# Optimization experiments

Measured on AMD Instinct MI355X. Metric: run time of the kernel, lower is better.

## Reference

```python
import jax, jax.numpy as jnp
import numpy as np

BN_EPS = 1e-3  # Keras BatchNormalization default epsilon
K = 7          # kernel_size


def setup_inputs() -> dict:
    key = jax.random.key(0)
    ks = jax.random.split(key, 5)
    B, L, C, F = 128, 512, 128, 128
    L_out = L - K + 1  # 506, valid padding, stride 1
    x = jax.random.normal(ks[0], (B, L, C), dtype=jnp.float32)
    # LocallyConnected1D unshared weights: (L_out, K*C, F), lecun_normal ~ N(0, 1/fan_in)
    kernel = jax.random.normal(ks[1], (L_out, K * C, F), dtype=jnp.float32) * (1.0 / np.sqrt(K * C))
    bias = jnp.zeros((L_out, F), dtype=jnp.float32)
    gamma = jnp.ones((F,), dtype=jnp.float32)
    beta = jnp.zeros((F,), dtype=jnp.float32)
    moving_mean = jax.random.normal(ks[2], (F,), dtype=jnp.float32) * 0.1
    moving_var = jax.random.uniform(ks[3], (F,), dtype=jnp.float32, minval=0.5, maxval=1.5)
    return {"x": x, "kernel": kernel, "bias": bias, "gamma": gamma,
            "beta": beta, "moving_mean": moving_mean, "moving_var": moving_var}


def _local_block(x, kernel, bias, gamma, beta, moving_mean, moving_var):
    B, L, C = x.shape
    L_out = L - K + 1
    F = kernel.shape[-1]
    # Patch extraction: idx[l, k] = l + k -> patches (B, L_out, K, C)
    idx = jnp.arange(L_out)[:, None] + jnp.arange(K)[None, :]
    patches = x[:, idx, :]                                  # (B, L_out, K, C)
    w = kernel.reshape(L_out, K, C, F)                      # unshared per-position weights
    y = jnp.einsum('blkc,lkcf->blf', patches, w) + bias     # (B, L_out, F)
    # BatchNorm (inference, axis=-1) fused with affine
    inv = gamma * jax.lax.rsqrt(moving_var + BN_EPS)
    y = y * inv + (beta - moving_mean * inv)
    return jax.nn.relu(y)


def reference(x, kernel, bias, gamma, beta, moving_mean, moving_var):
    return _local_block(x, kernel, bias, gamma, beta, moving_mean, moving_var)
```

## Files before the change

### kernel.cpp

```cpp
#include <hip/hip_runtime.h>

#define LO 506
#define LL 512
#define CC 128
#define FF 128
#define KC 896
#define BK 32
#define NK 28
#define XS 40
#define WS 40

typedef __attribute__((ext_vector_type(8))) short short8;
typedef __attribute__((ext_vector_type(4))) float floatx4;
typedef __attribute__((ext_vector_type(4))) unsigned int uintx4;
typedef unsigned short ushort_t;

static __device__ __forceinline__ ushort_t f2bf(float f) {
    union { float f; unsigned int u; } c; c.f = f;
    unsigned int u = c.u;
    return (ushort_t)((u + 0x7fffu + ((u >> 16) & 1u)) >> 16);
}
static __device__ __forceinline__ unsigned int pk2(float a, float b) {
    return (unsigned int)f2bf(a) | ((unsigned int)f2bf(b) << 16);
}

__global__ __launch_bounds__(512, 4)
void local_block_kernel(const float* __restrict__ x,
                        const float* __restrict__ wg,
                        const float* __restrict__ bias,
                        const float* __restrict__ gamma,
                        const float* __restrict__ beta,
                        const float* __restrict__ mmean,
                        const float* __restrict__ mvar,
                        float* __restrict__ out)
{
    const int l    = blockIdx.x;
    const int t    = threadIdx.x;
    const int lane = t & 63;
    const int wave = t >> 6;
    const int q    = lane >> 4;
    const int l16  = lane & 15;
    const int wr   = wave >> 1;
    const int wc   = wave & 1;

    __shared__ __align__(16) ushort_t Xs[128 * XS];
    __shared__ __align__(16) ushort_t Wt[128 * WS];

    const int am  = t >> 2;
    const int ak0 = (t & 3) * 8;
    const float* aptr = x + (size_t)am * (LL * CC) + l * CC + ak0;
    ushort_t* asd = &Xs[am * XS + ak0];

    const int wf  = t & 127;
    const int wk  = (t >> 7) * 8;
    const float* wptr = wg + (size_t)l * (KC * FF) + wf;
    ushort_t* wsd = &Wt[wf * WS + wk];

    floatx4 acc[2][4] = {};

    floatx4 areg[2];
    float   wreg[8];

#define LOAD_A(KT) { const float* p = aptr + (KT) * BK;                         \
        areg[0] = *(const floatx4*)(p);                                         \
        areg[1] = *(const floatx4*)(p + 4); }

#define LOAD_W(KT) { const float* p = wptr + (size_t)((KT) * BK + wk) * FF;     \
        _Pragma("unroll") for (int j = 0; j < 8; ++j)                           \
            wreg[j] = __builtin_nontemporal_load(p + j * FF); }

    LOAD_A(0); LOAD_W(0);

    for (int kt = 0; kt < NK; ++kt) {
        __syncthreads();
        {
            uintx4 av = { pk2(areg[0].x, areg[0].y),
                          pk2(areg[0].z, areg[0].w),
                          pk2(areg[1].x, areg[1].y),
                          pk2(areg[1].z, areg[1].w) };
            *(uintx4*)asd = av;
        }
        {
            uintx4 wv = { pk2(wreg[0], wreg[1]),
                          pk2(wreg[2], wreg[3]),
                          pk2(wreg[4], wreg[5]),
                          pk2(wreg[6], wreg[7]) };
            *(uintx4*)wsd = wv;
        }
        __syncthreads();
        if (kt + 1 < NK) { LOAD_A(kt + 1); LOAD_W(kt + 1); }
        short8 af[2], bfr[4];
#pragma unroll
        for (int mi = 0; mi < 2; ++mi)
            af[mi] = *(const short8*)&Xs[(wr*32 + mi*16 + l16) * XS + q*8];
#pragma unroll
        for (int ni = 0; ni < 4; ++ni)
            bfr[ni] = *(const short8*)&Wt[(wc*64 + ni*16 + l16) * WS + q*8];
#pragma unroll
        for (int mi = 0; mi < 2; ++mi)
#pragma unroll
            for (int ni = 0; ni < 4; ++ni)
                acc[mi][ni] = __builtin_amdgcn_mfma_f32_16x16x32_bf16(
                    af[mi], bfr[ni], acc[mi][ni], 0, 0, 0);
    }

#pragma unroll
    for (int ni = 0; ni < 4; ++ni) {
        int f = wc*64 + ni*16 + l16;
        float inv = gamma[f] * rsqrtf(mvar[f] + 1e-3f);
        float off = bias[l * FF + f] * inv + beta[f] - mmean[f] * inv;
#pragma unroll
        for (int mi = 0; mi < 2; ++mi) {
#pragma unroll
            for (int rg = 0; rg < 4; ++rg) {
                int b = wr*32 + mi*16 + q*4 + rg;
                float v = acc[mi][ni][rg] * inv + off;
                __builtin_nontemporal_store(fmaxf(v, 0.0f),
                    &out[((size_t)b * LO + l) * FF + f]);
            }
        }
    }
#undef LOAD_A
#undef LOAD_W
}

extern "C" void kernel_launch(void* const* d_in, const int* in_sizes, int n_in,
                              void* d_out, int out_size, void* d_ws, size_t ws_size,
                              hipStream_t stream) {
    const float* x     = (const float*)d_in[0];
    const float* w     = (const float*)d_in[1];
    const float* bias  = (const float*)d_in[2];
    const float* gamma = (const float*)d_in[3];
    const float* beta  = (const float*)d_in[4];
    const float* mmean = (const float*)d_in[5];
    const float* mvar  = (const float*)d_in[6];
    float* out = (float*)d_out;

    local_block_kernel<<<dim3(LO), dim3(512), 0, stream>>>(
        x, w, bias, gamma, beta, mmean, mvar, out);
}
```

Baseline: 361.1 us.

## Double-buffer LDS tiles with two-deep register prefetch and XCD-aware block remap

Switches to two LDS buffers and two register prefetch sets, so global loads for tile k+2 are in flight while tile k is computed. This leaves one barrier per k-step instead of two. It also remaps block IDs so that consecutive positions l land on the same XCD, which should improve L2 sharing of the overlapping x rows. The cost is more registers and twice the LDS, which may reduce occupancy. The barrier relies on the alternating buffers to avoid write-after-read hazards.

```diff
diff --git a/kernel.cpp b/kernel.cpp
--- a/kernel.cpp
+++ b/kernel.cpp
@@ -34,7 +34,14 @@
                         const float* __restrict__ mvar,
                         float* __restrict__ out)
 {
-    const int l    = blockIdx.x;
+    const int bid = blockIdx.x;
+    const int xcd = bid & 7;
+    const int idx = bid >> 3;
+    const int q8  = LO >> 3;
+    const int r8  = LO & 7;
+    const int l   = (xcd < r8) ? xcd * (q8 + 1) + idx
+                               : r8 * (q8 + 1) + (xcd - r8) * q8 + idx;
+
     const int t    = threadIdx.x;
     const int lane = t & 63;
     const int wave = t >> 6;
@@ -43,65 +50,66 @@
     const int wr   = wave >> 1;
     const int wc   = wave & 1;
 
-    __shared__ __align__(16) ushort_t Xs[128 * XS];
-    __shared__ __align__(16) ushort_t Wt[128 * WS];
+    __shared__ __align__(16) ushort_t Xs[2][128 * XS];
+    __shared__ __align__(16) ushort_t Wt[2][128 * WS];
 
     const int am  = t >> 2;
     const int ak0 = (t & 3) * 8;
     const float* aptr = x + (size_t)am * (LL * CC) + l * CC + ak0;
-    ushort_t* asd = &Xs[am * XS + ak0];
 
     const int wf  = t & 127;
     const int wk  = (t >> 7) * 8;
     const float* wptr = wg + (size_t)l * (KC * FF) + wf;
-    ushort_t* wsd = &Wt[wf * WS + wk];
 
     floatx4 acc[2][4] = {};
 
-    floatx4 areg[2];
-    float   wreg[8];
+    floatx4 areg0[2], areg1[2];
+    float   wreg0[8], wreg1[8];
 
-#define LOAD_A(KT) { const float* p = aptr + (KT) * BK;                         \
-        areg[0] = *(const floatx4*)(p);                                         \
-        areg[1] = *(const floatx4*)(p + 4); }
+#define LOAD_A(AR, KT) { const float* p = aptr + (KT) * BK;                     \
+        AR[0] = *(const floatx4*)(p);                                           \
+        AR[1] = *(const floatx4*)(p + 4); }
 
-#define LOAD_W(KT) { const float* p = wptr + (size_t)((KT) * BK + wk) * FF;     \
+#define LOAD_W(WR, KT) { const float* p = wptr + (size_t)((KT) * BK + wk) * FF; \
         _Pragma("unroll") for (int j = 0; j < 8; ++j)                           \
-            wreg[j] = __builtin_nontemporal_load(p + j * FF); }
+            WR[j] = __builtin_nontemporal_load(p + j * FF); }
 
-    LOAD_A(0); LOAD_W(0);
+#define STAGE(S, AR, WR) {                                                      \
+        uintx4 av = { pk2(AR[0].x, AR[0].y), pk2(AR[0].z, AR[0].w),             \
+                      pk2(AR[1].x, AR[1].y), pk2(AR[1].z, AR[1].w) };           \
+        *(uintx4*)&Xs[S][am * XS + ak0] = av;                                   \
+        uintx4 wv = { pk2(WR[0], WR[1]), pk2(WR[2], WR[3]),                     \
+                      pk2(WR[4], WR[5]), pk2(WR[6], WR[7]) };                   \
+        *(uintx4*)&Wt[S][wf * WS + wk] = wv; }
 
-    for (int kt = 0; kt < NK; ++kt) {
-        __syncthreads();
-        {
-            uintx4 av = { pk2(areg[0].x, areg[0].y),
-                          pk2(areg[0].z, areg[0].w),
-                          pk2(areg[1].x, areg[1].y),
-                          pk2(areg[1].z, areg[1].w) };
-            *(uintx4*)asd = av;
-        }
-        {
-            uintx4 wv = { pk2(wreg[0], wreg[1]),
-                          pk2(wreg[2], wreg[3]),
-                          pk2(wreg[4], wreg[5]),
-                          pk2(wreg[6], wreg[7]) };
-            *(uintx4*)wsd = wv;
-        }
-        __syncthreads();
-        if (kt + 1 < NK) { LOAD_A(kt + 1); LOAD_W(kt + 1); }
-        short8 af[2], bfr[4];
-#pragma unroll
-        for (int mi = 0; mi < 2; ++mi)
-            af[mi] = *(const short8*)&Xs[(wr*32 + mi*16 + l16) * XS + q*8];
-#pragma unroll
-        for (int ni = 0; ni < 4; ++ni)
-            bfr[ni] = *(const short8*)&Wt[(wc*64 + ni*16 + l16) * WS + q*8];
-#pragma unroll
-        for (int mi = 0; mi < 2; ++mi)
-#pragma unroll
-            for (int ni = 0; ni < 4; ++ni)
-                acc[mi][ni] = __builtin_amdgcn_mfma_f32_16x16x32_bf16(
-                    af[mi], bfr[ni], acc[mi][ni], 0, 0, 0);
+#define BAR() {                                                                 \
+        asm volatile("s_waitcnt lgkmcnt(0)" ::: "memory");                      \
+        __builtin_amdgcn_s_barrier();                                           \
+        asm volatile("" ::: "memory"); }
+
+#define COMPUTE(S) {                                                            \
+        short8 af[2], bfr[4];                                                   \
+        _Pragma("unroll") for (int mi = 0; mi < 2; ++mi)                        \
+            af[mi] = *(const short8*)&Xs[S][(wr*32 + mi*16 + l16) * XS + q*8];  \
+        _Pragma("unroll") for (int ni = 0; ni < 4; ++ni)                        \
+            bfr[ni] = *(const short8*)&Wt[S][(wc*64 + ni*16 + l16) * WS + q*8]; \
+        _Pragma("unroll") for (int mi = 0; mi < 2; ++mi)                        \
+            _Pragma("unroll") for (int ni = 0; ni < 4; ++ni)                    \
+                acc[mi][ni] = __builtin_amdgcn_mfma_f32_16x16x32_bf16(          \
+                    af[mi], bfr[ni], acc[mi][ni], 0, 0, 0); }
+
+    LOAD_A(areg0, 0); LOAD_W(wreg0, 0);
+    LOAD_A(areg1, 1); LOAD_W(wreg1, 1);
+
+    for (int kt = 0; kt < NK; kt += 2) {
+        STAGE(0, areg0, wreg0);
+        if (kt + 2 < NK) { LOAD_A(areg0, kt + 2); LOAD_W(wreg0, kt + 2); }
+        BAR();
+        COMPUTE(0);
+        STAGE(1, areg1, wreg1);
+        if (kt + 3 < NK) { LOAD_A(areg1, kt + 3); LOAD_W(wreg1, kt + 3); }
+        BAR();
+        COMPUTE(1);
     }
 
 #pragma unroll
@@ -122,6 +130,9 @@
     }
 #undef LOAD_A
 #undef LOAD_W
+#undef STAGE
+#undef BAR
+#undef COMPUTE
 }
 
 extern "C" void kernel_launch(void* const* d_in, const int* in_sizes, int n_in,
```

Result: faster. 347.2 us (-3.9%).
